# Optimization experiments

Measured on AMD Instinct MI355X. Metric: run time of the kernel, lower is better.

Reference implementation:

```python
import jax, jax.numpy as jnp
import numpy as np
from jax import lax

C = 256      # in_c == out_c == dim
NH = 8       # num_heads
K = 7        # depthwise pos-enc kernel
H1 = 512     # int(mlp_ratio * in_c) = 2.0 * 256
B, Hs, Ws = 2, 48, 48


def setup_inputs() -> dict:
    key = jax.random.key(0)
    ks = jax.random.split(key, 8)
    w = lambda k, shape: jax.random.normal(k, shape, jnp.float32) * 0.02
    return {
        "x": jax.random.normal(ks[0], (B, C, Hs, Ws), jnp.float32),
        # 1x1 convs stored as [out, in] (BN folded into weight+bias)
        "qk_w": w(ks[1], (2 * C, C)), "qk_b": jnp.zeros((2 * C,), jnp.float32),
        "v_w": w(ks[2], (C, C)),       "v_b": jnp.zeros((C,), jnp.float32),
        # depthwise positional encoding conv [C,1,K,K]
        "pe_w": w(ks[3], (C, 1, K, K)), "pe_b": jnp.zeros((C,), jnp.float32),
        "proj_w": w(ks[4], (C, C)),    "proj_b": jnp.zeros((C,), jnp.float32),
        # conv FFN: 1x1 (SiLU) -> 1x1 (no act)
        "fc1_w": w(ks[5], (H1, C)),    "fc1_b": jnp.zeros((H1,), jnp.float32),
        "fc2_w": w(ks[6], (C, H1)),    "fc2_b": jnp.zeros((C,), jnp.float32),
    }


def _c1(x, w, b):
    # 1x1 conv == per-pixel matmul
    return jnp.einsum('bchw,oc->bohw', x, w) + b[None, :, None, None]


def reference(x, qk_w, qk_b, v_w, v_b, pe_w, pe_b, proj_w, proj_b,
              fc1_w, fc1_b, fc2_w, fc2_b):
    Bb, Cc, Hh, Ww = x.shape
    hd = Cc // NH                 # head_dim = 32
    N = Hh * Ww
    scale = hd ** -0.5

    # ---- AttentionV2 ----
    qk = _c1(x, qk_w, qk_b).reshape(Bb, NH, 2 * hd, N)
    q, k = qk[:, :, :hd], qk[:, :, hd:]
    v_full = _c1(x, v_w, v_b)                      # [B,C,H,W]
    pe = lax.conv_general_dilated(
        v_full, pe_w, (1, 1), 'SAME', feature_group_count=Cc,
        dimension_numbers=('NCHW', 'OIHW', 'NCHW')) + pe_b[None, :, None, None]
    v = v_full.reshape(Bb, NH, hd, N)

    # attn = q^T @ k * scale ; softmax over keys
    attn = jax.nn.softmax(jnp.einsum('bhdn,bhdm->bhnm', q, k) * scale, axis=-1)
    o = jnp.einsum('bhdm,bhnm->bhdn', v, attn).reshape(Bb, Cc, Hh, Ww)
    attn_out = _c1(o + pe, proj_w, proj_b)

    # ---- block residuals + conv FFN (add=True) ----
    x1 = x + attn_out
    h = jax.nn.silu(_c1(x1, fc1_w, fc1_b))         # Conv(in_c, hidden, 1, 1) with SiLU
    return x1 + _c1(h, fc2_w, fc2_b)               # Conv(hidden, out_c, 1, act=False)
```

## Files before the change

kernel.cpp:

```cpp
#include <hip/hip_runtime.h>
#include <hip/hip_bf16.h>

#define NCH 256
#define NHD 8
#define HD 32
#define NPIX 2304
#define H1DIM 512

typedef __attribute__((ext_vector_type(8))) __bf16 bf16x8;
typedef __attribute__((ext_vector_type(4))) float f32x4;

__global__ __launch_bounds__(256) void prep_k(
    const float* __restrict__ x,
    const float* __restrict__ w0, const float* __restrict__ w1,
    const float* __restrict__ w2, const float* __restrict__ w3,
    const float* __restrict__ w4,
    __bf16* __restrict__ Xb, __bf16* __restrict__ Wall) {
    const int tid = threadIdx.x;
    if (blockIdx.x < 288) {
        const int t = blockIdx.x;
        const int b = t / 144, r0 = t % 144;
        const int c0 = (r0 / 36) * 64, n0 = (r0 % 36) * 64;
        __shared__ float tile[64][65];
        const size_t sb = ((size_t)b * NCH + c0) * NPIX + n0;
#pragma unroll
        for (int i = 0; i < 16; ++i) {
            int idx = tid + i * 256;
            int rr = idx >> 6, cc = idx & 63;
            tile[rr][cc] = x[sb + (size_t)rr * NPIX + cc];
        }
        __syncthreads();
#pragma unroll
        for (int i = 0; i < 8; ++i) {
            int idx = tid + i * 256;
            int nn = idx >> 5, cp = (idx & 31) * 2;
            union { __bf16 h[2]; unsigned u; } pk;
            pk.h[0] = (__bf16)tile[cp][nn];
            pk.h[1] = (__bf16)tile[cp + 1][nn];
            *(unsigned*)&Xb[((size_t)b * NPIX + n0 + nn) * NCH + c0 + cp] = pk.u;
        }
    } else {
        int i = (blockIdx.x - 288) * 256 + tid;
        const float* src; int off;
        if (i < 32768)      { src = w0; off = i; }
        else if (i < 49152) { src = w1; off = i - 32768; }
        else if (i < 65536) { src = w2; off = i - 49152; }
        else if (i < 98304) { src = w3; off = i - 65536; }
        else                { src = w4; off = i - 98304; }
        float4 v = ((const float4*)src)[off];
        union { __bf16 h[4]; uint2 u; } pk;
        pk.h[0] = (__bf16)v.x; pk.h[1] = (__bf16)v.y;
        pk.h[2] = (__bf16)v.z; pk.h[3] = (__bf16)v.w;
        ((uint2*)Wall)[i] = pk.u;
    }
}

__global__ __launch_bounds__(256) void qkv_k(
    const __bf16* __restrict__ A, const __bf16* __restrict__ Wq,
    const __bf16* __restrict__ Wv, const float* __restrict__ qk_b,
    const float* __restrict__ v_b, __bf16* __restrict__ Qb,
    __bf16* __restrict__ Kf, float* __restrict__ v_bu,
    __bf16* __restrict__ Vf) {
    const int tid = threadIdx.x;
    const int wave = tid >> 6, lane = tid & 63;
    const int l16 = lane & 15, quad = lane >> 4;
    const int h = blockIdx.x & 7;
    const int u = blockIdx.x >> 3;
    const int tau = u * 4 + wave;
    const int px = tau % 144;
    const int rest = tau / 144;
    const int b = rest & 1;
    const int sub = rest >> 1;
    const int m0 = px * 16;
    const bool isv = sub >= 4;
    const int oc0 = isv ? (32 * h + 16 * (sub - 4)) : (64 * h + 16 * sub);
    const __bf16* W = isv ? Wv : Wq;

    const __bf16* aptr = A + ((size_t)b * NPIX + m0 + l16) * NCH + quad * 8;
    const __bf16* bptr = W + (size_t)(oc0 + l16) * NCH + quad * 8;

    f32x4 acc = {0.f, 0.f, 0.f, 0.f};
#pragma unroll 8
    for (int k = 0; k < NCH; k += 32) {
        bf16x8 af = *(const bf16x8*)(aptr + k);
        bf16x8 bf = *(const bf16x8*)(bptr + k);
        acc = __builtin_amdgcn_mfma_f32_16x16x32_bf16(af, bf, acc, 0, 0, 0);
    }

    const int oc = oc0 + l16;
    const int mb = m0 + quad * 4;

    if (!isv) {
        const float bb = qk_b[oc];
        const int bh = b * NHD + h;
        const int dd = (oc0 & 16) + l16;
        if ((oc0 & 32) == 0) {
            const float qs = 0.17677669529663689f * 1.4426950408889634f;
#pragma unroll
            for (int r = 0; r < 4; ++r)
                Qb[((size_t)bh * NPIX + mb + r) * 32 + dd] = (__bf16)((acc[r] + bb) * qs);
        } else {
            __bf16* kp = Kf + ((size_t)(bh * 144 + px) * 64 + (dd >> 3) * 16 + quad * 4) * 8 + (dd & 7);
#pragma unroll
            for (int r = 0; r < 4; ++r) kp[r * 8] = (__bf16)(acc[r] + bb);
        }
    } else {
        const float bb = v_b[oc];
        const int bh = b * NHD + h;
        const int half = (oc0 >> 4) & 1;
        const size_t fb = ((size_t)b * NCH + oc) * NPIX + mb;
        float4 vf_; float* vp = &vf_.x;
        union { __bf16 hh[4]; uint2 u; } pk;
#pragma unroll
        for (int r = 0; r < 4; ++r) {
            float v = acc[r] + bb;
            vp[r] = v; pk.hh[r] = (__bf16)v;
        }
        *(float4*)&v_bu[fb] = vf_;
        *(uint2*)&Vf[((size_t)(bh * 144 + px) * 64 + lane) * 8 + half * 4] = pk.u;
    }
}

__global__ __launch_bounds__(512) void attn7_k(const __bf16* __restrict__ Qb,
                                               const __bf16* __restrict__ Kf,
                                               const __bf16* __restrict__ Vf,
                                               const float* __restrict__ v_bu,
                                               const float* __restrict__ pe_w,
                                               const float* __restrict__ pe_b,
                                               __bf16* __restrict__ opb) {
    const int tid = threadIdx.x;
    const int wave = tid >> 6, lane = tid & 63;
    const int l16 = lane & 15, quad = lane >> 4;
    const int h = blockIdx.x & 7;
    const int r0 = (int)blockIdx.x >> 3;
    const int qt = r0 % 72;
    const int b = r0 / 72;
    const int qb = qt * 32;
    const int bh = b * NHD + h;

    __shared__ float o_s[8][32][33];
    __shared__ float l_s[8][32];

    bf16x8 b_q0 = *(const bf16x8*)(Qb + ((size_t)bh * NPIX + qb + l16) * 32 + quad * 8);
    bf16x8 b_q1 = *(const bf16x8*)(Qb + ((size_t)bh * NPIX + qb + 16 + l16) * 32 + quad * 8);

    const __bf16* kf = Kf + ((size_t)(bh * 144 + wave * 18) * 64 + lane) * 8;
    const __bf16* vf = Vf + ((size_t)(bh * 144 + wave * 18) * 64 + lane) * 8;

    f32x4 o00 = {0.f,0.f,0.f,0.f}, o01 = {0.f,0.f,0.f,0.f};
    f32x4 o10 = {0.f,0.f,0.f,0.f}, o11 = {0.f,0.f,0.f,0.f};
    f32x4 l0 = {0.f,0.f,0.f,0.f}, l1 = {0.f,0.f,0.f,0.f};

#pragma unroll 3
    for (int t = 0; t < 18; ++t) {
        bf16x8 a_k = *(const bf16x8*)(kf + (size_t)t * 512);
        bf16x8 va  = *(const bf16x8*)(vf + (size_t)t * 512);
        f32x4 z = {0.f, 0.f, 0.f, 0.f};
        f32x4 s0 = __builtin_amdgcn_mfma_f32_16x16x32_bf16(a_k, b_q0, z, 0, 0, 0);
        f32x4 s1 = __builtin_amdgcn_mfma_f32_16x16x32_bf16(a_k, b_q1, z, 0, 0, 0);
        f32x4 p0, p1;
#pragma unroll
        for (int r = 0; r < 4; ++r) {
            p0[r] = __builtin_amdgcn_exp2f(s0[r]);
            p1[r] = __builtin_amdgcn_exp2f(s1[r]);
        }
        l0 += p0; l1 += p1;
        bf16x8 b0lo = {}, b0hi = {}, b1lo = {}, b1hi = {};
#pragma unroll
        for (int r = 0; r < 4; ++r) {
            __bf16 c0 = (__bf16)p0[r], c1 = (__bf16)p1[r];
            b0lo[r] = c0; b0hi[4 + r] = c0;
            b1lo[r] = c1; b1hi[4 + r] = c1;
        }
        o00 = __builtin_amdgcn_mfma_f32_16x16x32_bf16(va, b0lo, o00, 0, 0, 0);
        o01 = __builtin_amdgcn_mfma_f32_16x16x32_bf16(va, b0hi, o01, 0, 0, 0);
        o10 = __builtin_amdgcn_mfma_f32_16x16x32_bf16(va, b1lo, o10, 0, 0, 0);
        o11 = __builtin_amdgcn_mfma_f32_16x16x32_bf16(va, b1hi, o11, 0, 0, 0);
    }

    float ls0 = l0[0] + l0[1] + l0[2] + l0[3];
    ls0 += __shfl_xor(ls0, 16); ls0 += __shfl_xor(ls0, 32);
    float ls1 = l1[0] + l1[1] + l1[2] + l1[3];
    ls1 += __shfl_xor(ls1, 16); ls1 += __shfl_xor(ls1, 32);

#pragma unroll
    for (int r = 0; r < 4; ++r) {
        o_s[wave][quad * 4 + r][l16]           = o00[r];
        o_s[wave][16 + quad * 4 + r][l16]      = o01[r];
        o_s[wave][quad * 4 + r][16 + l16]      = o10[r];
        o_s[wave][16 + quad * 4 + r][16 + l16] = o11[r];
    }
    if (quad == 0) { l_s[wave][l16] = ls0; l_s[wave][16 + l16] = ls1; }
    __syncthreads();

    const int q = tid & 31;
    const int d0 = (tid >> 5) * 2;
    float l = 0.f;
#pragma unroll
    for (int w = 0; w < 8; ++w) l += l_s[w][q];
    const float inv = 1.f / l;
    float v0 = 0.f, v1 = 0.f;
#pragma unroll
    for (int w = 0; w < 8; ++w) {
        v0 += o_s[w][d0][q];
        v1 += o_s[w][d0 + 1][q];
    }
    const int n = qb + q;
    const int ch = h * HD + d0;

    const int y = n / 48, x0 = n - y * 48;
    const size_t vb0 = ((size_t)b * NCH + ch) * NPIX;
    const float* wk0 = pe_w + ch * 49;
    const float* wk1 = wk0 + 49;
    float pe0 = pe_b[ch], pe1 = pe_b[ch + 1];
#pragma unroll
    for (int ky = 0; ky < 7; ++ky) {
        int yy = y + ky - 3;
        if ((unsigned)yy < 48u) {
#pragma unroll
            for (int kx = 0; kx < 7; ++kx) {
                int xx = x0 + kx - 3;
                if ((unsigned)xx < 48u) {
                    const int off = yy * 48 + xx;
                    pe0 += wk0[ky * 7 + kx] * v_bu[vb0 + off];
                    pe1 += wk1[ky * 7 + kx] * v_bu[vb0 + NPIX + off];
                }
            }
        }
    }

    v0 = v0 * inv + pe0;
    v1 = v1 * inv + pe1;
    union { __bf16 hh[2]; unsigned u; } pk;
    pk.hh[0] = (__bf16)v0; pk.hh[1] = (__bf16)v1;
    *(unsigned*)&opb[((size_t)b * NPIX + n) * NCH + ch] = pk.u;
}

__global__ __launch_bounds__(512, 2) void mlp_k(
    const __bf16* __restrict__ opb, const __bf16* __restrict__ Wp,
    const __bf16* __restrict__ W1, const __bf16* __restrict__ W2,
    const float* __restrict__ pj_b, const float* __restrict__ f1_b,
    const float* __restrict__ f2_b, const float* __restrict__ x,
    float* __restrict__ out) {
    const int tid = threadIdx.x;
    const int wave = tid >> 6, lane = tid & 63;
    const int l16 = lane & 15, quad = lane >> 4;
    const int b = (int)blockIdx.x / 144;
    const int m0 = ((int)blockIdx.x % 144) * 16;

    __shared__ __bf16 x1h[16][264];
    __shared__ __bf16 hh[16][520];

    const int oc_a = wave * 16 + l16;
    const int oc_b = oc_a + 128;
    const int row = quad * 4;
    const int mq = m0 + quad * 4;

    const __bf16* aptr = opb + ((size_t)b * NPIX + m0 + l16) * NCH + quad * 8;
    const __bf16* wp0 = Wp + (size_t)oc_a * NCH + quad * 8;
    const __bf16* wp1 = Wp + (size_t)oc_b * NCH + quad * 8;
    f32x4 a0 = {0.f, 0.f, 0.f, 0.f}, a1 = {0.f, 0.f, 0.f, 0.f};
#pragma unroll
    for (int k = 0; k < NCH; k += 32) {
        bf16x8 af = *(const bf16x8*)(aptr + k);
        a0 = __builtin_amdgcn_mfma_f32_16x16x32_bf16(af, *(const bf16x8*)(wp0 + k), a0, 0, 0, 0);
        a1 = __builtin_amdgcn_mfma_f32_16x16x32_bf16(af, *(const bf16x8*)(wp1 + k), a1, 0, 0, 0);
    }
    float x1r0[4], x1r1[4];
    {
        const float bb0 = pj_b[oc_a], bb1 = pj_b[oc_b];
        float4 xr0 = *(const float4*)&x[((size_t)b * NCH + oc_a) * NPIX + mq];
        float4 xr1 = *(const float4*)&x[((size_t)b * NCH + oc_b) * NPIX + mq];
        const float* xp0 = &xr0.x;
        const float* xp1 = &xr1.x;
#pragma unroll
        for (int r = 0; r < 4; ++r) {
            float v0 = a0[r] + bb0 + xp0[r];
            float v1 = a1[r] + bb1 + xp1[r];
            x1r0[r] = v0; x1r1[r] = v1;
            x1h[row + r][oc_a] = (__bf16)v0;
            x1h[row + r][oc_b] = (__bf16)v1;
        }
    }
    __syncthreads();

    {
        const __bf16* w10 = W1 + (size_t)oc_a * NCH + quad * 8;
        const __bf16* w11 = W1 + (size_t)(oc_a + 128) * NCH + quad * 8;
        const __bf16* w12 = W1 + (size_t)(oc_a + 256) * NCH + quad * 8;
        const __bf16* w13 = W1 + (size_t)(oc_a + 384) * NCH + quad * 8;
        f32x4 c0 = {0.f, 0.f, 0.f, 0.f}, c1 = {0.f, 0.f, 0.f, 0.f};
        f32x4 c2 = {0.f, 0.f, 0.f, 0.f}, c3 = {0.f, 0.f, 0.f, 0.f};
#pragma unroll
        for (int k = 0; k < NCH; k += 32) {
            bf16x8 af = *(const bf16x8*)&x1h[l16][quad * 8 + k];
            c0 = __builtin_amdgcn_mfma_f32_16x16x32_bf16(af, *(const bf16x8*)(w10 + k), c0, 0, 0, 0);
            c1 = __builtin_amdgcn_mfma_f32_16x16x32_bf16(af, *(const bf16x8*)(w11 + k), c1, 0, 0, 0);
            c2 = __builtin_amdgcn_mfma_f32_16x16x32_bf16(af, *(const bf16x8*)(w12 + k), c2, 0, 0, 0);
            c3 = __builtin_amdgcn_mfma_f32_16x16x32_bf16(af, *(const bf16x8*)(w13 + k), c3, 0, 0, 0);
        }
        const float g0 = f1_b[oc_a], g1 = f1_b[oc_a + 128];
        const float g2 = f1_b[oc_a + 256], g3 = f1_b[oc_a + 384];
#pragma unroll
        for (int r = 0; r < 4; ++r) {
            float v0 = c0[r] + g0; v0 = v0 / (1.f + __expf(-v0));
            float v1 = c1[r] + g1; v1 = v1 / (1.f + __expf(-v1));
            float v2 = c2[r] + g2; v2 = v2 / (1.f + __expf(-v2));
            float v3 = c3[r] + g3; v3 = v3 / (1.f + __expf(-v3));
            hh[row + r][oc_a]       = (__bf16)v0;
            hh[row + r][oc_a + 128] = (__bf16)v1;
            hh[row + r][oc_a + 256] = (__bf16)v2;
            hh[row + r][oc_a + 384] = (__bf16)v3;
        }
    }
    __syncthreads();

    {
        const __bf16* w20 = W2 + (size_t)oc_a * H1DIM + quad * 8;
        const __bf16* w21 = W2 + (size_t)oc_b * H1DIM + quad * 8;
        f32x4 d0 = {0.f, 0.f, 0.f, 0.f}, d1 = {0.f, 0.f, 0.f, 0.f};
#pragma unroll
        for (int k = 0; k < H1DIM; k += 32) {
            bf16x8 af = *(const bf16x8*)&hh[l16][quad * 8 + k];
            d0 = __builtin_amdgcn_mfma_f32_16x16x32_bf16(af, *(const bf16x8*)(w20 + k), d0, 0, 0, 0);
            d1 = __builtin_amdgcn_mfma_f32_16x16x32_bf16(af, *(const bf16x8*)(w21 + k), d1, 0, 0, 0);
        }
        const float g0 = f2_b[oc_a], g1 = f2_b[oc_b];
        float4 o0, o1;
        float* p0 = &o0.x; float* p1 = &o1.x;
#pragma unroll
        for (int r = 0; r < 4; ++r) {
            p0[r] = d0[r] + g0 + x1r0[r];
            p1[r] = d1[r] + g1 + x1r1[r];
        }
        *(float4*)&out[((size_t)b * NCH + oc_a) * NPIX + mq] = o0;
        *(float4*)&out[((size_t)b * NCH + oc_b) * NPIX + mq] = o1;
    }
}

extern "C" void kernel_launch(void* const* d_in, const int* in_sizes, int n_in,
                              void* d_out, int out_size, void* d_ws, size_t ws_size,
                              hipStream_t stream) {
    const float* x    = (const float*)d_in[0];
    const float* qk_w = (const float*)d_in[1];
    const float* qk_b = (const float*)d_in[2];
    const float* v_w  = (const float*)d_in[3];
    const float* v_b  = (const float*)d_in[4];
    const float* pe_w = (const float*)d_in[5];
    const float* pe_b = (const float*)d_in[6];
    const float* pj_w = (const float*)d_in[7];
    const float* pj_b = (const float*)d_in[8];
    const float* f1_w = (const float*)d_in[9];
    const float* f1_b = (const float*)d_in[10];
    const float* f2_w = (const float*)d_in[11];
    const float* f2_b = (const float*)d_in[12];
    float* out = (float*)d_out;

    const int B = 2;
    const size_t plane = (size_t)NCH * NPIX;
    const size_t bp = (size_t)B * plane;

    float* v_bu  = (float*)d_ws;
    __bf16* Xb   = (__bf16*)(v_bu + bp);
    __bf16* opb  = Xb + bp;
    __bf16* Qb   = opb + bp;
    __bf16* Kf   = Qb + bp;
    __bf16* Vf   = Kf + bp;
    __bf16* Wall = Vf + bp;
    __bf16* Wq = Wall;
    __bf16* Wv = Wall + 131072;
    __bf16* Wp = Wall + 196608;
    __bf16* W1 = Wall + 262144;
    __bf16* W2 = Wall + 393216;

    prep_k<<<800, 256, 0, stream>>>(x, qk_w, v_w, pj_w, f1_w, f2_w, Xb, Wall);
    qkv_k<<<3456, 256, 0, stream>>>(Xb, Wq, Wv, qk_b, v_b, Qb, Kf, v_bu, Vf);
    attn7_k<<<1152, 512, 0, stream>>>(Qb, Kf, Vf, v_bu, pe_w, pe_b, opb);
    mlp_k<<<288, 512, 0, stream>>>(opb, Wp, W1, W2, pj_b, f1_b, f2_b, x, out);
}
```

Before: 192.8 us.

## Stage MLP weights into LDS via global_load_lds DMA with fragment-major activation layout

```diff
diff --git a/kernel.cpp b/kernel.cpp
--- a/kernel.cpp
+++ b/kernel.cpp
@@ -236,7 +236,28 @@
     *(unsigned*)&opb[((size_t)b * NPIX + n) * NCH + ch] = pk.u;
 }
 
-__global__ __launch_bounds__(512, 2) void mlp_k(
+__device__ __forceinline__ void stage_dma(const __bf16* __restrict__ src,
+                                          __bf16* lds_base) {
+    __builtin_amdgcn_global_load_lds(
+        (const __attribute__((address_space(1))) void*)(src),
+        (__attribute__((address_space(3))) void*)(lds_base), 16, 0, 0);
+}
+
+template <int ND>
+__device__ __forceinline__ void stage_tile(const __bf16* __restrict__ Wg,
+                                           int row0, int K, __bf16* lds_base,
+                                           int l16, int quad) {
+    const __bf16* src = Wg + (size_t)(row0 + l16) * K + quad * 8;
+#pragma unroll
+    for (int d = 0; d < ND; ++d)
+        stage_dma(src + d * 32, lds_base + d * 512);
+}
+
+__device__ __forceinline__ int fragidx(int ch, int pix) {
+    return ((ch >> 5) << 9) + (((ch >> 3) & 3) << 7) + (pix << 3) + (ch & 7);
+}
+
+__global__ __launch_bounds__(512) void mlp_k(
     const __bf16* __restrict__ opb, const __bf16* __restrict__ Wp,
     const __bf16* __restrict__ W1, const __bf16* __restrict__ W2,
     const float* __restrict__ pj_b, const float* __restrict__ f1_b,
@@ -248,29 +269,42 @@
     const int b = (int)blockIdx.x / 144;
     const int m0 = ((int)blockIdx.x % 144) * 16;
 
-    __shared__ __bf16 x1h[16][264];
-    __shared__ __bf16 hh[16][520];
-
-    const int oc_a = wave * 16 + l16;
+    __shared__ __bf16 Wb[65536];
+    __shared__ __bf16 x1f[4096];
+    __shared__ __bf16 hf[8192];
+
+    __bf16* reg0 = Wb + wave * 8192;
+    __bf16* reg1 = reg0 + 4096;
+
+    const int w16 = wave * 16;
+    const int oc_a = w16 + l16;
     const int oc_b = oc_a + 128;
-    const int row = quad * 4;
     const int mq = m0 + quad * 4;
 
+    stage_tile<8>(Wp, w16, NCH, reg0, l16, quad);
+    stage_tile<8>(Wp, w16 + 128, NCH, reg1, l16, quad);
     const __bf16* aptr = opb + ((size_t)b * NPIX + m0 + l16) * NCH + quad * 8;
-    const __bf16* wp0 = Wp + (size_t)oc_a * NCH + quad * 8;
-    const __bf16* wp1 = Wp + (size_t)oc_b * NCH + quad * 8;
+    bf16x8 afr[8];
+#pragma unroll
+    for (int i = 0; i < 8; ++i) afr[i] = *(const bf16x8*)(aptr + i * 32);
+    float4 xr0 = *(const float4*)&x[((size_t)b * NCH + oc_a) * NPIX + mq];
+    float4 xr1 = *(const float4*)&x[((size_t)b * NCH + oc_b) * NPIX + mq];
+    asm volatile("s_waitcnt vmcnt(0)" ::: "memory");
+
     f32x4 a0 = {0.f, 0.f, 0.f, 0.f}, a1 = {0.f, 0.f, 0.f, 0.f};
 #pragma unroll
-    for (int k = 0; k < NCH; k += 32) {
-        bf16x8 af = *(const bf16x8*)(aptr + k);
-        a0 = __builtin_amdgcn_mfma_f32_16x16x32_bf16(af, *(const bf16x8*)(wp0 + k), a0, 0, 0, 0);
-        a1 = __builtin_amdgcn_mfma_f32_16x16x32_bf16(af, *(const bf16x8*)(wp1 + k), a1, 0, 0, 0);
-    }
+    for (int k = 0; k < 8; ++k) {
+        bf16x8 w0 = *(const bf16x8*)(reg0 + k * 512 + lane * 8);
+        bf16x8 w1 = *(const bf16x8*)(reg1 + k * 512 + lane * 8);
+        a0 = __builtin_amdgcn_mfma_f32_16x16x32_bf16(afr[k], w0, a0, 0, 0, 0);
+        a1 = __builtin_amdgcn_mfma_f32_16x16x32_bf16(afr[k], w1, a1, 0, 0, 0);
+    }
+    stage_tile<8>(W1, w16, NCH, reg0, l16, quad);
+    stage_tile<8>(W1, w16 + 128, NCH, reg1, l16, quad);
+
     float x1r0[4], x1r1[4];
     {
         const float bb0 = pj_b[oc_a], bb1 = pj_b[oc_b];
-        float4 xr0 = *(const float4*)&x[((size_t)b * NCH + oc_a) * NPIX + mq];
-        float4 xr1 = *(const float4*)&x[((size_t)b * NCH + oc_b) * NPIX + mq];
         const float* xp0 = &xr0.x;
         const float* xp1 = &xr1.x;
 #pragma unroll
@@ -278,27 +312,37 @@
             float v0 = a0[r] + bb0 + xp0[r];
             float v1 = a1[r] + bb1 + xp1[r];
             x1r0[r] = v0; x1r1[r] = v1;
-            x1h[row + r][oc_a] = (__bf16)v0;
-            x1h[row + r][oc_b] = (__bf16)v1;
-        }
-    }
-    __syncthreads();
-
+            x1f[fragidx(oc_a, quad * 4 + r)] = (__bf16)v0;
+            x1f[fragidx(oc_b, quad * 4 + r)] = (__bf16)v1;
+        }
+    }
+    asm volatile("s_waitcnt lgkmcnt(0)" ::: "memory");
+    __builtin_amdgcn_s_barrier();
+
+    asm volatile("s_waitcnt vmcnt(0)" ::: "memory");
+    f32x4 c0 = {0.f, 0.f, 0.f, 0.f}, c1 = {0.f, 0.f, 0.f, 0.f};
+#pragma unroll
+    for (int k = 0; k < 8; ++k) {
+        bf16x8 xa = *(const bf16x8*)(x1f + k * 512 + lane * 8);
+        bf16x8 w0 = *(const bf16x8*)(reg0 + k * 512 + lane * 8);
+        bf16x8 w1 = *(const bf16x8*)(reg1 + k * 512 + lane * 8);
+        c0 = __builtin_amdgcn_mfma_f32_16x16x32_bf16(xa, w0, c0, 0, 0, 0);
+        c1 = __builtin_amdgcn_mfma_f32_16x16x32_bf16(xa, w1, c1, 0, 0, 0);
+    }
+    stage_tile<8>(W1, w16 + 256, NCH, reg0, l16, quad);
+    stage_tile<8>(W1, w16 + 384, NCH, reg1, l16, quad);
+    asm volatile("s_waitcnt vmcnt(0)" ::: "memory");
+    f32x4 c2 = {0.f, 0.f, 0.f, 0.f}, c3 = {0.f, 0.f, 0.f, 0.f};
+#pragma unroll
+    for (int k = 0; k < 8; ++k) {
+        bf16x8 xa = *(const bf16x8*)(x1f + k * 512 + lane * 8);
+        bf16x8 w0 = *(const bf16x8*)(reg0 + k * 512 + lane * 8);
+        bf16x8 w1 = *(const bf16x8*)(reg1 + k * 512 + lane * 8);
+        c2 = __builtin_amdgcn_mfma_f32_16x16x32_bf16(xa, w0, c2, 0, 0, 0);
+        c3 = __builtin_amdgcn_mfma_f32_16x16x32_bf16(xa, w1, c3, 0, 0, 0);
+    }
+    stage_tile<16>(W2, w16, H1DIM, reg0, l16, quad);
     {
-        const __bf16* w10 = W1 + (size_t)oc_a * NCH + quad * 8;
-        const __bf16* w11 = W1 + (size_t)(oc_a + 128) * NCH + quad * 8;
-        const __bf16* w12 = W1 + (size_t)(oc_a + 256) * NCH + quad * 8;
-        const __bf16* w13 = W1 + (size_t)(oc_a + 384) * NCH + quad * 8;
-        f32x4 c0 = {0.f, 0.f, 0.f, 0.f}, c1 = {0.f, 0.f, 0.f, 0.f};
-        f32x4 c2 = {0.f, 0.f, 0.f, 0.f}, c3 = {0.f, 0.f, 0.f, 0.f};
-#pragma unroll
-        for (int k = 0; k < NCH; k += 32) {
-            bf16x8 af = *(const bf16x8*)&x1h[l16][quad * 8 + k];
-            c0 = __builtin_amdgcn_mfma_f32_16x16x32_bf16(af, *(const bf16x8*)(w10 + k), c0, 0, 0, 0);
-            c1 = __builtin_amdgcn_mfma_f32_16x16x32_bf16(af, *(const bf16x8*)(w11 + k), c1, 0, 0, 0);
-            c2 = __builtin_amdgcn_mfma_f32_16x16x32_bf16(af, *(const bf16x8*)(w12 + k), c2, 0, 0, 0);
-            c3 = __builtin_amdgcn_mfma_f32_16x16x32_bf16(af, *(const bf16x8*)(w13 + k), c3, 0, 0, 0);
-        }
         const float g0 = f1_b[oc_a], g1 = f1_b[oc_a + 128];
         const float g2 = f1_b[oc_a + 256], g3 = f1_b[oc_a + 384];
 #pragma unroll
@@ -307,24 +351,34 @@
             float v1 = c1[r] + g1; v1 = v1 / (1.f + __expf(-v1));
             float v2 = c2[r] + g2; v2 = v2 / (1.f + __expf(-v2));
             float v3 = c3[r] + g3; v3 = v3 / (1.f + __expf(-v3));
-            hh[row + r][oc_a]       = (__bf16)v0;
-            hh[row + r][oc_a + 128] = (__bf16)v1;
-            hh[row + r][oc_a + 256] = (__bf16)v2;
-            hh[row + r][oc_a + 384] = (__bf16)v3;
-        }
-    }
-    __syncthreads();
-
+            const int pix = quad * 4 + r;
+            hf[fragidx(oc_a, pix)]       = (__bf16)v0;
+            hf[fragidx(oc_a + 128, pix)] = (__bf16)v1;
+            hf[fragidx(oc_a + 256, pix)] = (__bf16)v2;
+            hf[fragidx(oc_a + 384, pix)] = (__bf16)v3;
+        }
+    }
+    asm volatile("s_waitcnt lgkmcnt(0)" ::: "memory");
+    __builtin_amdgcn_s_barrier();
+
+    asm volatile("s_waitcnt vmcnt(0)" ::: "memory");
+    f32x4 d0 = {0.f, 0.f, 0.f, 0.f};
+#pragma unroll
+    for (int k = 0; k < 16; ++k) {
+        bf16x8 ha = *(const bf16x8*)(hf + k * 512 + lane * 8);
+        bf16x8 w0 = *(const bf16x8*)(reg0 + k * 512 + lane * 8);
+        d0 = __builtin_amdgcn_mfma_f32_16x16x32_bf16(ha, w0, d0, 0, 0, 0);
+    }
+    stage_tile<16>(W2, w16 + 128, H1DIM, reg0, l16, quad);
+    asm volatile("s_waitcnt vmcnt(0)" ::: "memory");
+    f32x4 d1 = {0.f, 0.f, 0.f, 0.f};
+#pragma unroll
+    for (int k = 0; k < 16; ++k) {
+        bf16x8 ha = *(const bf16x8*)(hf + k * 512 + lane * 8);
+        bf16x8 w0 = *(const bf16x8*)(reg0 + k * 512 + lane * 8);
+        d1 = __builtin_amdgcn_mfma_f32_16x16x32_bf16(ha, w0, d1, 0, 0, 0);
+    }
     {
-        const __bf16* w20 = W2 + (size_t)oc_a * H1DIM + quad * 8;
-        const __bf16* w21 = W2 + (size_t)oc_b * H1DIM + quad * 8;
-        f32x4 d0 = {0.f, 0.f, 0.f, 0.f}, d1 = {0.f, 0.f, 0.f, 0.f};
-#pragma unroll
-        for (int k = 0; k < H1DIM; k += 32) {
-            bf16x8 af = *(const bf16x8*)&hh[l16][quad * 8 + k];
-            d0 = __builtin_amdgcn_mfma_f32_16x16x32_bf16(af, *(const bf16x8*)(w20 + k), d0, 0, 0, 0);
-            d1 = __builtin_amdgcn_mfma_f32_16x16x32_bf16(af, *(const bf16x8*)(w21 + k), d1, 0, 0, 0);
-        }
         const float g0 = f2_b[oc_a], g1 = f2_b[oc_b];
         float4 o0, o1;
         float* p0 = &o0.x; float* p1 = &o1.x;
```

New measurement: 194.9 us. Within noise of the previous version (+1.1%).
